# Performance work log

Hardware: AMD Instinct MI355X
Metric: run time of the kernel (lower is better)

## Reference

```python
import jax, jax.numpy as jnp
import numpy as np

N_NODES, N_EDGES, H, Q, RBF = 10000, 160000, 128, 16, 32
CUTOFF_UPPER = 4.5


def tensor_norm(t):
    # Frobenius norm squared over the trailing 3x3 dims -> [n, h]
    return (t * t).sum((-2, -1))


def decompose_tensor(X):
    # X: [n, h, 3, 3] -> I: [n, h] (trace/3), A skew, S symmetric-traceless
    eye = jnp.eye(3, dtype=X.dtype)
    I = jnp.einsum('nhii->nh', X) / 3.0
    Xt = jnp.swapaxes(X, -1, -2)
    A = 0.5 * (X - Xt)
    S = 0.5 * (X + Xt) - I[..., None, None] * eye
    return I, A, S


def I_to_tensor(I):
    return I[..., None, None] * jnp.eye(3, dtype=I.dtype)


def skewtensor_to_vector(A):
    return jnp.stack((A[..., 2, 1], A[..., 0, 2], A[..., 1, 0]), axis=-1)


def vector_to_skewtensor(v):
    z = jnp.zeros_like(v[..., 0])
    rows = jnp.stack((z, -v[..., 2], v[..., 1],
                      v[..., 2], z, -v[..., 0],
                      -v[..., 1], v[..., 0], z), axis=-1)
    return rows.reshape(v.shape[:-1] + (3, 3))


def setup_inputs() -> dict:
    key = jax.random.key(0)
    ks = jax.random.split(key, 12)
    d_in = RBF + 2 * Q  # 64
    inp = {
        'X': jax.random.normal(ks[0], (N_NODES, H, 3, 3), jnp.float32),
        'charges': jax.random.normal(ks[1], (N_NODES, Q), jnp.float32),
        'edge_weight': jax.random.uniform(ks[2], (N_EDGES,), jnp.float32) * CUTOFF_UPPER,
        'edge_attr': jax.random.normal(ks[3], (N_EDGES, RBF), jnp.float32),
        'W1': jax.random.normal(ks[4], (d_in, H), jnp.float32) / np.sqrt(d_in),
        'b1': jnp.zeros((H,), jnp.float32),
        'W2': jax.random.normal(ks[5], (H, 2 * H), jnp.float32) / np.sqrt(H),
        'b2': jnp.zeros((2 * H,), jnp.float32),
        'W3': jax.random.normal(ks[6], (2 * H, 3 * H), jnp.float32) / np.sqrt(2 * H),
        'b3': jnp.zeros((3 * H,), jnp.float32),
        'Wt': jax.random.normal(ks[7], (6, H, H), jnp.float32) / np.sqrt(H),
        'edge_index': jax.random.randint(ks[8], (2, N_EDGES), 0, N_NODES, jnp.int64 if jax.config.jax_enable_x64 else jnp.int32),
    }
    return inp


def reference(X, charges, edge_weight, edge_attr, W1, b1, W2, b2, W3, b3, Wt, edge_index):
    n, h = X.shape[0], X.shape[1]
    src, dst = edge_index[0], edge_index[1]

    # CosineCutoff (cutoff_lower = 0)
    C = 0.5 * (jnp.cos(edge_weight * (jnp.pi / CUTOFF_UPPER)) + 1.0)
    C = C * (edge_weight < CUTOFF_UPPER).astype(X.dtype)

    # edge MLP on [edge_attr | charges_i | charges_j]
    x = jnp.concatenate([edge_attr, charges[src], charges[dst]], axis=-1)
    x = jax.nn.silu(x @ W1 + b1)
    x = jax.nn.silu(x @ W2 + b2)
    x = jax.nn.silu(x @ W3 + b3)
    x = (x * C[:, None]).reshape(-1, 3, h)  # [E, 3, h]

    # normalize node tensor features
    X = X / (tensor_norm(X) + 1.0)[..., None, None]
    I, A, S = decompose_tensor(X)
    I = I @ Wt[0]
    A = jnp.einsum('nhij,hg->ngij', A, Wt[1])
    S = jnp.einsum('nhij,hg->ngij', S, Wt[2])
    Y = A + S + I_to_tensor(I)

    # message passing: gather from dst node, scale by edge factor, scatter-add to src
    Im = jax.ops.segment_sum(x[:, 0, :] * I[dst], src, num_segments=n)
    Av = skewtensor_to_vector(A)
    Am_vec = jax.ops.segment_sum(x[:, 1, :, None] * Av[dst], src, num_segments=n)
    Sm = jax.ops.segment_sum(x[:, 2, :, None, None] * S[dst], src, num_segments=n)
    msg = vector_to_skewtensor(Am_vec) + Sm + I_to_tensor(Im)

    # O(3) recombination
    A2 = jnp.matmul(msg, Y)
    B2 = jnp.matmul(Y, msg)
    I, A, S = decompose_tensor(A2 + B2)

    _X = A + S + I_to_tensor(I)
    normp1 = tensor_norm(_X) + 1.0
    I = I / normp1
    A = A / normp1[..., None, None]
    S = S / normp1[..., None, None]
    I = I @ Wt[3]
    A = jnp.einsum('nhij,hg->ngij', A, Wt[4])
    S = jnp.einsum('nhij,hg->ngij', S, Wt[5])
    dX = A + S + I_to_tensor(I)

    return X + dX + jnp.matmul(dX, dX)
```

## Files before the change

### kernel.cpp

```cpp
#include <hip/hip_runtime.h>
#include <math.h>

#define NND 10000
#define NE  160000
#define HD  128
#define NH  (NND*HD)

typedef _Float16 f16;
typedef _Float16 half8 __attribute__((ext_vector_type(8)));
typedef float floatx4 __attribute__((ext_vector_type(4)));

__device__ __forceinline__ float silu_f(float v) {
    return v * (1.0f / (1.0f + __expf(-v)));
}

__global__ __launch_bounds__(256) void w_prep(const float* __restrict__ W1,
                                              const float* __restrict__ W2,
                                              const float* __restrict__ W3,
                                              const float* __restrict__ Wt,
                                              f16* __restrict__ w1t,
                                              f16* __restrict__ w2t,
                                              f16* __restrict__ w3t,
                                              f16* __restrict__ wtT) {
    int id = blockIdx.x * 256 + threadIdx.x;
    if (id < 128*64) { int n = id >> 6, k = id & 63;  w1t[id] = (f16)W1[k*128 + n]; return; }
    id -= 128*64;
    if (id < 256*128) { int n = id >> 7, k = id & 127; w2t[id] = (f16)W2[k*256 + n]; return; }
    id -= 256*128;
    if (id < 384*256) { int n = id >> 8, k = id & 255; w3t[id] = (f16)W3[k*384 + n]; return; }
    id -= 384*256;
    if (id < 6*128*128) {
        int wi = id >> 14, rem = id & 16383;
        int n = rem >> 7, k = rem & 127;
        wtT[(size_t)wi*16384 + n*128 + k] = (f16)Wt[(size_t)wi*16384 + k*128 + n];
    }
}

__global__ __launch_bounds__(256) void hist_kernel(const int* __restrict__ eidx,
                                                   int* __restrict__ hist) {
    int e = blockIdx.x * 256 + threadIdx.x;
    if (e < NE) atomicAdd(&hist[eidx[e]], 1);
}

__global__ __launch_bounds__(1024) void scan_kernel(const int* __restrict__ hist,
                                                    int* __restrict__ offs,
                                                    int* __restrict__ cursor) {
    __shared__ int sums[1024];
    int t = threadIdx.x;
    int base = t * 10;
    int loc[10]; int s = 0;
    #pragma unroll
    for (int i = 0; i < 10; i++) {
        int v = (base + i < NND) ? hist[base + i] : 0;
        loc[i] = s; s += v;
    }
    sums[t] = s;
    __syncthreads();
    for (int off = 1; off < 1024; off <<= 1) {
        int v = (t >= off) ? sums[t - off] : 0;
        __syncthreads();
        sums[t] += v;
        __syncthreads();
    }
    int basesum = (t > 0) ? sums[t - 1] : 0;
    #pragma unroll
    for (int i = 0; i < 10; i++)
        if (base + i < NND) { offs[base + i] = basesum + loc[i]; cursor[base + i] = basesum + loc[i]; }
}

__global__ __launch_bounds__(256) void scatter_kernel(const int* __restrict__ eidx,
                                                      int* __restrict__ cursor,
                                                      int* __restrict__ perm,
                                                      int* __restrict__ ssrc,
                                                      int* __restrict__ sdst) {
    int e = blockIdx.x * 256 + threadIdx.x;
    if (e >= NE) return;
    int s = eidx[e], d = eidx[NE + e];
    int pos = atomicAdd(&cursor[s], 1);
    perm[pos] = e; ssrc[pos] = s; sdst[pos] = d;
}

__global__ __launch_bounds__(256) void node_prep(const float* __restrict__ X,
                                                 f16* __restrict__ comp) {
    int idx = blockIdx.x * 256 + threadIdx.x;
    if (idx >= NH) return;
    const float* xp = X + (size_t)idx * 9;
    float x[9];
    #pragma unroll
    for (int i = 0; i < 9; i++) x[i] = xp[i];
    float nsq = 0.f;
    #pragma unroll
    for (int i = 0; i < 9; i++) nsq = fmaf(x[i], x[i], nsq);
    float inv = 1.0f / (nsq + 1.0f);
    #pragma unroll
    for (int i = 0; i < 9; i++) x[i] *= inv;

    float I0  = (x[0] + x[4] + x[8]) * (1.0f / 3.0f);
    float a0  = 0.5f * (x[7] - x[5]);
    float a1  = 0.5f * (x[2] - x[6]);
    float a2  = 0.5f * (x[3] - x[1]);
    float s00 = x[0] - I0;
    float s11 = x[4] - I0;
    float s22 = x[8] - I0;
    float s01 = 0.5f * (x[1] + x[3]);
    float s02 = 0.5f * (x[2] + x[6]);
    float s12 = 0.5f * (x[5] + x[7]);

    comp[0*NH + idx] = (f16)I0;
    comp[1*NH + idx] = (f16)a0;  comp[2*NH + idx] = (f16)a1;  comp[3*NH + idx] = (f16)a2;
    comp[4*NH + idx] = (f16)s00; comp[5*NH + idx] = (f16)s11; comp[6*NH + idx] = (f16)s22;
    comp[7*NH + idx] = (f16)s01; comp[8*NH + idx] = (f16)s02; comp[9*NH + idx] = (f16)s12;
}

__global__ __launch_bounds__(256) void mix_mfma(const f16* __restrict__ A,
                                                const f16* __restrict__ WtT,
                                                float* __restrict__ C,
                                                f16* __restrict__ Ch,
                                                int w0, int w1, int w2, int writeCh) {
    const int g = blockIdx.y;
    const int baseRow = (g == 0) ? 0   : (g == 1 ? NND   : 4*NND);
    const int Mg      = (g == 0) ? NND : (g == 1 ? 3*NND : 6*NND);
    const int row0 = blockIdx.x * 64;
    if (row0 >= Mg) return;
    const int wi = (g == 0) ? w0 : (g == 1 ? w1 : w2);
    const f16* B = WtT + (size_t)wi * 128 * 128;

    __shared__ f16 As[64 * 136];

    const int t = threadIdx.x;
    const int l = t & 63, wid = t >> 6, lr = l & 15, lh = l >> 4;

    #pragma unroll
    for (int i = 0; i < 4; i++) {
        int id = t + 256 * i;
        int r = id >> 4, ch = id & 15;
        int rr = row0 + r; if (rr >= Mg) rr = Mg - 1;
        *(half8*)&As[r*136 + ch*8] =
            *(const half8*)&A[((size_t)baseRow + rr) * HD + ch*8];
    }
    __syncthreads();

    floatx4 acc[8];
    #pragma unroll
    for (int n = 0; n < 8; n++) acc[n] = (floatx4)0.0f;

    #pragma unroll
    for (int k0 = 0; k0 < 128; k0 += 32) {
        half8 a = *(const half8*)&As[(wid*16 + lr)*136 + k0 + lh*8];
        #pragma unroll
        for (int n = 0; n < 8; n++) {
            half8 b = *(const half8*)&B[(size_t)(n*16 + lr)*128 + k0 + lh*8];
            acc[n] = __builtin_amdgcn_mfma_f32_16x16x32_f16(a, b, acc[n], 0, 0, 0);
        }
    }

    #pragma unroll
    for (int n = 0; n < 8; n++) {
        #pragma unroll
        for (int r = 0; r < 4; r++) {
            int gl = row0 + wid*16 + lh*4 + r;
            if (gl < Mg) {
                size_t grow = (size_t)baseRow + gl;
                int col = n*16 + lr;
                float val = acc[n][r];
                C[grow * HD + col] = val;
                if (writeCh) {
                    int plane = (int)(grow / NND);
                    int node  = (int)(grow - (size_t)plane * NND);
                    Ch[((size_t)node * 10 + plane) * HD + col] = (f16)val;
                }
            }
        }
    }
}

__global__ __launch_bounds__(256, 3) void edge_mlp_v(
    const float* __restrict__ edge_attr, const float* __restrict__ charges,
    const float* __restrict__ edge_weight,
    const int* __restrict__ offs,
    const int* __restrict__ perm, const int* __restrict__ ssrc, const int* __restrict__ sdst,
    const f16* __restrict__ W1t, const float* __restrict__ b1,
    const f16* __restrict__ W2t, const float* __restrict__ b2,
    const f16* __restrict__ W3t, const float* __restrict__ b3,
    f16* __restrict__ vbuf, int n0, int n1, int VC)
{
    __shared__ __align__(16) char pool[51200];
    f16* x1s = (f16*)pool;
    f16* x2s = (f16*)(pool + 17408);
    f16* x0s = x2s;
    f16* stage = (f16*)pool;

    __shared__ int   srcS[64];
    __shared__ int   dstS[64];
    __shared__ int   permS[64];
    __shared__ float Cs[64];

    const int pbase = offs[n0];
    const int pend  = (n1 >= NND) ? NE : offs[n1];
    const int eb    = blockIdx.x * 64;
    if (pbase + eb >= pend) return;

    const int t   = threadIdx.x;
    const int l   = t & 63;
    const int wid = t >> 6;
    const int lr  = l & 15;
    const int lh  = l >> 4;

    if (t < 64) {
        int pe = pbase + eb + t;
        if (pe > NE - 1) pe = NE - 1;
        int eo = perm[pe];
        permS[t] = eo;
        srcS[t]  = ssrc[pe];
        dstS[t]  = sdst[pe];
        float w = edge_weight[eo];
        float c = 0.5f * (cosf(w * (float)(M_PI / 4.5)) + 1.0f);
        Cs[t] = (w < 4.5f) ? c : 0.0f;
    }
    __syncthreads();

    #pragma unroll
    for (int i = 0; i < 16; i++) {
        int lin = t + 256 * i;
        int e = lin >> 6, col = lin & 63;
        float v;
        if (col < 32)      v = edge_attr[(size_t)permS[e] * 32 + col];
        else if (col < 48) v = charges[(size_t)srcS[e] * 16 + (col - 32)];
        else               v = charges[(size_t)dstS[e] * 16 + (col - 48)];
        x0s[e * 72 + col] = (f16)v;
    }
    __syncthreads();

    {
        floatx4 acc[2][4];
        #pragma unroll
        for (int n = 0; n < 2; n++)
            #pragma unroll
            for (int m = 0; m < 4; m++) acc[n][m] = (floatx4)0.0f;

        #pragma unroll
        for (int k0 = 0; k0 < 64; k0 += 32) {
            half8 a[4];
            #pragma unroll
            for (int m = 0; m < 4; m++)
                a[m] = *(const half8*)&x0s[(m*16 + lr)*72 + k0 + lh*8];
            #pragma unroll
            for (int n = 0; n < 2; n++) {
                int colb = wid*32 + n*16 + lr;
                half8 b = *(const half8*)&W1t[(size_t)colb*64 + k0 + lh*8];
                #pragma unroll
                for (int m = 0; m < 4; m++)
                    acc[n][m] = __builtin_amdgcn_mfma_f32_16x16x32_f16(a[m], b, acc[n][m], 0, 0, 0);
            }
        }
        __syncthreads();
        #pragma unroll
        for (int n = 0; n < 2; n++) {
            int col = wid*32 + n*16 + lr;
            float bb = b1[col];
            #pragma unroll
            for (int m = 0; m < 4; m++)
                #pragma unroll
                for (int r = 0; r < 4; r++) {
                    int row = m*16 + lh*4 + r;
                    x1s[row*136 + col] = (f16)silu_f(acc[n][m][r] + bb);
                }
        }
    }
    __syncthreads();

    {
        floatx4 acc[4][4];
        #pragma unroll
        for (int n = 0; n < 4; n++)
            #pragma unroll
            for (int m = 0; m < 4; m++) acc[n][m] = (floatx4)0.0f;

        #pragma unroll
        for (int k0 = 0; k0 < 128; k0 += 32) {
            half8 a[4];
            #pragma unroll
            for (int m = 0; m < 4; m++)
                a[m] = *(const half8*)&x1s[(m*16 + lr)*136 + k0 + lh*8];
            #pragma unroll
            for (int n = 0; n < 4; n++) {
                int colb = wid*64 + n*16 + lr;
                half8 b = *(const half8*)&W2t[(size_t)colb*128 + k0 + lh*8];
                #pragma unroll
                for (int m = 0; m < 4; m++)
                    acc[n][m] = __builtin_amdgcn_mfma_f32_16x16x32_f16(a[m], b, acc[n][m], 0, 0, 0);
            }
        }
        #pragma unroll
        for (int n = 0; n < 4; n++) {
            int col = wid*64 + n*16 + lr;
            float bb = b2[col];
            #pragma unroll
            for (int m = 0; m < 4; m++)
                #pragma unroll
                for (int r = 0; r < 4; r++) {
                    int row = m*16 + lh*4 + r;
                    x2s[row*264 + col] = (f16)silu_f(acc[n][m][r] + bb);
                }
        }
    }
    __syncthreads();

    floatx4 acc[6][4];
    #pragma unroll
    for (int n = 0; n < 6; n++)
        #pragma unroll
        for (int m = 0; m < 4; m++) acc[n][m] = (floatx4)0.0f;

    #pragma unroll
    for (int k0 = 0; k0 < 256; k0 += 32) {
        half8 a[4];
        #pragma unroll
        for (int m = 0; m < 4; m++)
            a[m] = *(const half8*)&x2s[(m*16 + lr)*264 + k0 + lh*8];
        #pragma unroll
        for (int n = 0; n < 6; n++) {
            int colb = wid*96 + n*16 + lr;
            half8 b = *(const half8*)&W3t[(size_t)colb*256 + k0 + lh*8];
            #pragma unroll
            for (int m = 0; m < 4; m++)
                acc[n][m] = __builtin_amdgcn_mfma_f32_16x16x32_f16(a[m], b, acc[n][m], 0, 0, 0);
        }
    }
    __syncthreads();

    #pragma unroll
    for (int n = 0; n < 6; n++) {
        int col = wid*96 + n*16 + lr;
        int g = col >> 7, h = col & 127;
        float bb = b3[col];
        #pragma unroll
        for (int m = 0; m < 4; m++)
            #pragma unroll
            for (int r = 0; r < 4; r++) {
                int e = m*16 + lh*4 + r;
                stage[e*392 + g*128 + h] = (f16)(silu_f(acc[n][m][r] + bb) * Cs[e]);
            }
    }
    __syncthreads();

    #pragma unroll
    for (int i = 0; i < 12; i++) {
        int c = t + 256 * i;
        int e = c / 48, j = c - e * 48;
        int g = j >> 4, h0 = (j & 15) * 8;
        half8 v = *(const half8*)&stage[e*392 + j*8];
        *(half8*)&vbuf[((size_t)g*VC + (size_t)(eb + e))*HD + h0] = v;
    }
}

__global__ __launch_bounds__(128) void scatter_combine(
    const int* __restrict__ offs, const int* __restrict__ ends,
    const int* __restrict__ sdst, const f16* __restrict__ vbuf,
    const f16* __restrict__ Ych, const float* __restrict__ Yc,
    f16* __restrict__ pre, int n0, int VC)
{
    const int s = n0 + blockIdx.x;
    const int h = threadIdx.x;
    const int pbase = offs[n0];
    const int p0 = offs[s], p1 = ends[s];

    float ps[10];
    #pragma unroll
    for (int c = 0; c < 10; c++) ps[c] = 0.f;

    int p = p0;
    for (; p + 1 < p1; p += 2) {
        int sl0 = p - pbase, sl1 = sl0 + 1;
        int d0 = sdst[p], d1 = sdst[p + 1];
        const f16* y0 = Ych + (size_t)d0 * 1280 + h;
        const f16* y1 = Ych + (size_t)d1 * 1280 + h;
        float va0 = (float)vbuf[((size_t)0*VC + sl0)*HD + h];
        float vb0 = (float)vbuf[((size_t)1*VC + sl0)*HD + h];
        float vc0 = (float)vbuf[((size_t)2*VC + sl0)*HD + h];
        float va1 = (float)vbuf[((size_t)0*VC + sl1)*HD + h];
        float vb1 = (float)vbuf[((size_t)1*VC + sl1)*HD + h];
        float vc1 = (float)vbuf[((size_t)2*VC + sl1)*HD + h];
        float y0r[10], y1r[10];
        #pragma unroll
        for (int c = 0; c < 10; c++) { y0r[c] = (float)y0[c*HD]; y1r[c] = (float)y1[c*HD]; }
        ps[0] = fmaf(va0, y0r[0], ps[0]);
        #pragma unroll
        for (int c = 1; c < 4; c++)  ps[c] = fmaf(vb0, y0r[c], ps[c]);
        #pragma unroll
        for (int c = 4; c < 10; c++) ps[c] = fmaf(vc0, y0r[c], ps[c]);
        ps[0] = fmaf(va1, y1r[0], ps[0]);
        #pragma unroll
        for (int c = 1; c < 4; c++)  ps[c] = fmaf(vb1, y1r[c], ps[c]);
        #pragma unroll
        for (int c = 4; c < 10; c++) ps[c] = fmaf(vc1, y1r[c], ps[c]);
    }
    if (p < p1) {
        int sl0 = p - pbase;
        int d0 = sdst[p];
        const f16* y0 = Ych + (size_t)d0 * 1280 + h;
        float va0 = (float)vbuf[((size_t)0*VC + sl0)*HD + h];
        float vb0 = (float)vbuf[((size_t)1*VC + sl0)*HD + h];
        float vc0 = (float)vbuf[((size_t)2*VC + sl0)*HD + h];
        float y0r[10];
        #pragma unroll
        for (int c = 0; c < 10; c++) y0r[c] = (float)y0[c*HD];
        ps[0] = fmaf(va0, y0r[0], ps[0]);
        #pragma unroll
        for (int c = 1; c < 4; c++)  ps[c] = fmaf(vb0, y0r[c], ps[c]);
        #pragma unroll
        for (int c = 4; c < 10; c++) ps[c] = fmaf(vc0, y0r[c], ps[c]);
    }

    const size_t idx = (size_t)s * HD + h;
    float yI  = Yc[0*(size_t)NH + idx];
    float ya0 = Yc[1*(size_t)NH + idx], ya1 = Yc[2*(size_t)NH + idx], ya2 = Yc[3*(size_t)NH + idx];
    float ys00 = Yc[4*(size_t)NH + idx], ys11 = Yc[5*(size_t)NH + idx], ys22 = Yc[6*(size_t)NH + idx];
    float ys01 = Yc[7*(size_t)NH + idx], ys02 = Yc[8*(size_t)NH + idx], ys12 = Yc[9*(size_t)NH + idx];

    float M[3][3] = {
        { ps[0] + ps[4],  ps[7] - ps[3],  ps[8] + ps[2] },
        { ps[7] + ps[3],  ps[0] + ps[5],  ps[9] - ps[1] },
        { ps[8] - ps[2],  ps[9] + ps[1],  ps[0] + ps[6] } };
    float Y[3][3] = {
        { yI + ys00,  ys01 - ya2, ys02 + ya1 },
        { ys01 + ya2, yI + ys11,  ys12 - ya0 },
        { ys02 - ya1, ys12 + ya0, yI + ys22  } };

    float T[3][3];
    #pragma unroll
    for (int r = 0; r < 3; r++)
        #pragma unroll
        for (int c = 0; c < 3; c++) {
            float acc = 0.f;
            #pragma unroll
            for (int k = 0; k < 3; k++)
                acc += M[r][k] * Y[k][c] + Y[r][k] * M[k][c];
            T[r][c] = acc;
        }

    float tr3 = (T[0][0] + T[1][1] + T[2][2]) * (1.0f / 3.0f);
    float nsq = 0.f;
    #pragma unroll
    for (int r = 0; r < 3; r++)
        #pragma unroll
        for (int c = 0; c < 3; c++) nsq = fmaf(T[r][c], T[r][c], nsq);
    float inv = 1.0f / (nsq + 1.0f);

    pre[0*(size_t)NH + idx] = (f16)(tr3 * inv);
    pre[1*(size_t)NH + idx] = (f16)(0.5f * (T[2][1] - T[1][2]) * inv);
    pre[2*(size_t)NH + idx] = (f16)(0.5f * (T[0][2] - T[2][0]) * inv);
    pre[3*(size_t)NH + idx] = (f16)(0.5f * (T[1][0] - T[0][1]) * inv);
    pre[4*(size_t)NH + idx] = (f16)((T[0][0] - tr3) * inv);
    pre[5*(size_t)NH + idx] = (f16)((T[1][1] - tr3) * inv);
    pre[6*(size_t)NH + idx] = (f16)((T[2][2] - tr3) * inv);
    pre[7*(size_t)NH + idx] = (f16)(0.5f * (T[0][1] + T[1][0]) * inv);
    pre[8*(size_t)NH + idx] = (f16)(0.5f * (T[0][2] + T[2][0]) * inv);
    pre[9*(size_t)NH + idx] = (f16)(0.5f * (T[1][2] + T[2][1]) * inv);
}

__global__ __launch_bounds__(256) void final_out(const float* __restrict__ post,
                                                 const float* __restrict__ X,
                                                 float* __restrict__ out) {
    int idx = blockIdx.x * 256 + threadIdx.x;
    if (idx >= NH) return;

    float dI  = post[0*NH + idx];
    float da0 = post[1*NH + idx], da1 = post[2*NH + idx], da2 = post[3*NH + idx];
    float ds00 = post[4*NH + idx], ds11 = post[5*NH + idx], ds22 = post[6*NH + idx];
    float ds01 = post[7*NH + idx], ds02 = post[8*NH + idx], ds12 = post[9*NH + idx];

    float D[3][3] = {
        { dI + ds00,  ds01 - da2, ds02 + da1 },
        { ds01 + da2, dI + ds11,  ds12 - da0 },
        { ds02 - da1, ds12 + da0, dI + ds22  } };

    const float* xp = X + (size_t)idx * 9;
    float x[9];
    #pragma unroll
    for (int i = 0; i < 9; i++) x[i] = xp[i];
    float nsq = 0.f;
    #pragma unroll
    for (int i = 0; i < 9; i++) nsq = fmaf(x[i], x[i], nsq);
    float inv = 1.0f / (nsq + 1.0f);

    float* op = out + (size_t)idx * 9;
    #pragma unroll
    for (int r = 0; r < 3; r++)
        #pragma unroll
        for (int c = 0; c < 3; c++) {
            float p = 0.f;
            #pragma unroll
            for (int k = 0; k < 3; k++) p = fmaf(D[r][k], D[k][c], p);
            op[r*3 + c] = x[r*3 + c] * inv + D[r][c] + p;
        }
}

extern "C" void kernel_launch(void* const* d_in, const int* in_sizes, int n_in,
                              void* d_out, int out_size, void* d_ws, size_t ws_size,
                              hipStream_t stream) {
    const float* X       = (const float*)d_in[0];
    const float* charges = (const float*)d_in[1];
    const float* ew      = (const float*)d_in[2];
    const float* ea      = (const float*)d_in[3];
    const float* W1      = (const float*)d_in[4];
    const float* b1      = (const float*)d_in[5];
    const float* W2      = (const float*)d_in[6];
    const float* b2      = (const float*)d_in[7];
    const float* W3      = (const float*)d_in[8];
    const float* b3      = (const float*)d_in[9];
    const float* Wt      = (const float*)d_in[10];
    const int*   eidx    = (const int*)d_in[11];
    float* out = (float*)d_out;

    float* f32a  = (float*)d_ws;
    f16*   fh16  = (f16*)(f32a + (size_t)10 * NH);
    f16*   ych   = fh16 + (size_t)10 * NH;
    f16*   w1t   = ych + (size_t)10 * NH;
    f16*   w2t   = w1t + 128*64;
    f16*   w3t   = w2t + 256*128;
    f16*   wtT   = w3t + 384*256;
    int*   hist   = (int*)(wtT + 6*128*128);
    int*   offs   = hist + NND;
    int*   cursor = offs + NND;
    int*   perm   = cursor + NND;
    int*   ssrc   = perm + NE;
    int*   sdst   = ssrc + NE;
    f16*   vbuf   = (f16*)(sdst + NE);

    size_t used = (size_t)((char*)vbuf - (char*)d_ws);
    int Q, VC;
    if      (used + (size_t)160000 * 384 * 2 <= ws_size) { Q = 1; VC = 160000; }
    else if (used + (size_t) 84480 * 384 * 2 <= ws_size) { Q = 2; VC = 84480;  }
    else if (used + (size_t) 48000 * 384 * 2 <= ws_size) { Q = 4; VC = 48000;  }
    else                                                 { Q = 8; VC = 24320;  }

    hipMemsetAsync(hist, 0, NND * sizeof(int), stream);

    w_prep<<<928, 256, 0, stream>>>(W1, W2, W3, Wt, w1t, w2t, w3t, wtT);
    node_prep<<<NH / 256, 256, 0, stream>>>(X, fh16);

    hist_kernel<<<(NE + 255) / 256, 256, 0, stream>>>(eidx, hist);
    scan_kernel<<<1, 1024, 0, stream>>>(hist, offs, cursor);
    scatter_kernel<<<(NE + 255) / 256, 256, 0, stream>>>(eidx, cursor, perm, ssrc, sdst);

    dim3 gmix((6 * NND + 63) / 64, 3);
    mix_mfma<<<gmix, 256, 0, stream>>>(fh16, wtT, f32a, ych, 0, 1, 2, 1);

    const int nodesPer = NND / Q;
    for (int q = 0; q < Q; q++) {
        int n0 = q * nodesPer, n1 = n0 + nodesPer;
        edge_mlp_v<<<VC / 64, 256, 0, stream>>>(ea, charges, ew, offs,
                                                perm, ssrc, sdst,
                                                w1t, b1, w2t, b2, w3t, b3,
                                                vbuf, n0, n1, VC);
        scatter_combine<<<nodesPer, 128, 0, stream>>>(offs, cursor, sdst, vbuf,
                                                      ych, f32a, fh16, n0, VC);
    }

    mix_mfma<<<gmix, 256, 0, stream>>>(fh16, wtT, f32a, ych, 3, 4, 5, 0);

    final_out<<<NH / 256, 256, 0, stream>>>(f32a, X, out);
}
```

Measured before the change: 423.6 us.

## Shrink edge MLP tile to 32 edges, swap MFMA operands, interleave vbuf layout

The edge MLP kernel now processes 32 edges per block instead of 64. That halves shared memory and accumulator registers, so launch bounds can rise from 3 to 6 blocks per SM. MFMA operands are swapped so weights are the A operand, which lets epilogue stores and bias loads be written as 4-wide vectors. The input gather uses float4 loads, and vbuf switches from plane-major to per-edge interleaved 384-wide rows so edge writes and combine reads stay contiguous. The cost is half the weight reuse per block and twice as many blocks re-reading the W matrices from global or L2 memory.

```diff
diff --git a/kernel.cpp b/kernel.cpp
--- a/kernel.cpp
+++ b/kernel.cpp
@@ -8,6 +8,7 @@
 
 typedef _Float16 f16;
 typedef _Float16 half8 __attribute__((ext_vector_type(8)));
+typedef _Float16 half4 __attribute__((ext_vector_type(4)));
 typedef float floatx4 __attribute__((ext_vector_type(4)));
 
 __device__ __forceinline__ float silu_f(float v) {
@@ -174,7 +175,7 @@
     }
 }
 
-__global__ __launch_bounds__(256, 3) void edge_mlp_v(
+__global__ __launch_bounds__(256, 6) void edge_mlp_v(
     const float* __restrict__ edge_attr, const float* __restrict__ charges,
     const float* __restrict__ edge_weight,
     const int* __restrict__ offs,
@@ -184,20 +185,20 @@
     const f16* __restrict__ W3t, const float* __restrict__ b3,
     f16* __restrict__ vbuf, int n0, int n1, int VC)
 {
-    __shared__ __align__(16) char pool[51200];
+    __shared__ __align__(16) char pool[25600];
     f16* x1s = (f16*)pool;
-    f16* x2s = (f16*)(pool + 17408);
+    f16* x2s = (f16*)(pool + 8704);
     f16* x0s = x2s;
     f16* stage = (f16*)pool;
 
-    __shared__ int   srcS[64];
-    __shared__ int   dstS[64];
-    __shared__ int   permS[64];
-    __shared__ float Cs[64];
+    __shared__ int   srcS[32];
+    __shared__ int   dstS[32];
+    __shared__ int   permS[32];
+    __shared__ float Cs[32];
 
     const int pbase = offs[n0];
     const int pend  = (n1 >= NND) ? NE : offs[n1];
-    const int eb    = blockIdx.x * 64;
+    const int eb    = blockIdx.x * 32;
     if (pbase + eb >= pend) return;
 
     const int t   = threadIdx.x;
@@ -206,7 +207,7 @@
     const int lr  = l & 15;
     const int lh  = l >> 4;
 
-    if (t < 64) {
+    if (t < 32) {
         int pe = pbase + eb + t;
         if (pe > NE - 1) pe = NE - 1;
         int eo = perm[pe];
@@ -219,138 +220,144 @@
     }
     __syncthreads();
 
-    #pragma unroll
-    for (int i = 0; i < 16; i++) {
-        int lin = t + 256 * i;
-        int e = lin >> 6, col = lin & 63;
-        float v;
-        if (col < 32)      v = edge_attr[(size_t)permS[e] * 32 + col];
-        else if (col < 48) v = charges[(size_t)srcS[e] * 16 + (col - 32)];
-        else               v = charges[(size_t)dstS[e] * 16 + (col - 48)];
-        x0s[e * 72 + col] = (f16)v;
-    }
-    __syncthreads();
-
     {
-        floatx4 acc[2][4];
+        int e = t >> 3, q = t & 7;
+        float4 va = *(const float4*)&edge_attr[(size_t)permS[e] * 32 + q * 4];
+        half4 ha; ha[0]=(f16)va.x; ha[1]=(f16)va.y; ha[2]=(f16)va.z; ha[3]=(f16)va.w;
+        *(half4*)&x0s[e*72 + q*4] = ha;
+        float4 vc; int col;
+        if (q < 4) { vc = *(const float4*)&charges[(size_t)srcS[e]*16 + q*4]; col = 32 + q*4; }
+        else       { vc = *(const float4*)&charges[(size_t)dstS[e]*16 + (q-4)*4]; col = 48 + (q-4)*4; }
+        half4 hc; hc[0]=(f16)vc.x; hc[1]=(f16)vc.y; hc[2]=(f16)vc.z; hc[3]=(f16)vc.w;
+        *(half4*)&x0s[e*72 + col] = hc;
+    }
+    __syncthreads();
+
+    {
+        floatx4 acc[2][2];
         #pragma unroll
         for (int n = 0; n < 2; n++)
             #pragma unroll
-            for (int m = 0; m < 4; m++) acc[n][m] = (floatx4)0.0f;
+            for (int m = 0; m < 2; m++) acc[n][m] = (floatx4)0.0f;
 
         #pragma unroll
         for (int k0 = 0; k0 < 64; k0 += 32) {
-            half8 a[4];
-            #pragma unroll
-            for (int m = 0; m < 4; m++)
-                a[m] = *(const half8*)&x0s[(m*16 + lr)*72 + k0 + lh*8];
+            half8 b[2];
+            #pragma unroll
+            for (int m = 0; m < 2; m++)
+                b[m] = *(const half8*)&x0s[(m*16 + lr)*72 + k0 + lh*8];
             #pragma unroll
             for (int n = 0; n < 2; n++) {
-                int colb = wid*32 + n*16 + lr;
-                half8 b = *(const half8*)&W1t[(size_t)colb*64 + k0 + lh*8];
+                half8 a = *(const half8*)&W1t[(size_t)(wid*32 + n*16 + lr)*64 + k0 + lh*8];
                 #pragma unroll
-                for (int m = 0; m < 4; m++)
-                    acc[n][m] = __builtin_amdgcn_mfma_f32_16x16x32_f16(a[m], b, acc[n][m], 0, 0, 0);
+                for (int m = 0; m < 2; m++)
+                    acc[n][m] = __builtin_amdgcn_mfma_f32_16x16x32_f16(a, b[m], acc[n][m], 0, 0, 0);
             }
         }
         __syncthreads();
         #pragma unroll
         for (int n = 0; n < 2; n++) {
-            int col = wid*32 + n*16 + lr;
-            float bb = b1[col];
-            #pragma unroll
-            for (int m = 0; m < 4; m++)
+            int col0 = wid*32 + n*16 + lh*4;
+            float4 bb = *(const float4*)&b1[col0];
+            #pragma unroll
+            for (int m = 0; m < 2; m++) {
+                int e = m*16 + lr;
+                half4 hv;
+                hv[0] = (f16)silu_f(acc[n][m][0] + bb.x);
+                hv[1] = (f16)silu_f(acc[n][m][1] + bb.y);
+                hv[2] = (f16)silu_f(acc[n][m][2] + bb.z);
+                hv[3] = (f16)silu_f(acc[n][m][3] + bb.w);
+                *(half4*)&x1s[e*136 + col0] = hv;
+            }
+        }
+    }
+    __syncthreads();
+
+    {
+        floatx4 acc[4][2];
+        #pragma unroll
+        for (int n = 0; n < 4; n++)
+            #pragma unroll
+            for (int m = 0; m < 2; m++) acc[n][m] = (floatx4)0.0f;
+
+        #pragma unroll
+        for (int k0 = 0; k0 < 128; k0 += 32) {
+            half8 b[2];
+            #pragma unroll
+            for (int m = 0; m < 2; m++)
+                b[m] = *(const half8*)&x1s[(m*16 + lr)*136 + k0 + lh*8];
+            #pragma unroll
+            for (int n = 0; n < 4; n++) {
+                half8 a = *(const half8*)&W2t[(size_t)(wid*64 + n*16 + lr)*128 + k0 + lh*8];
                 #pragma unroll
-                for (int r = 0; r < 4; r++) {
-                    int row = m*16 + lh*4 + r;
-                    x1s[row*136 + col] = (f16)silu_f(acc[n][m][r] + bb);
-                }
-        }
-    }
-    __syncthreads();
-
-    {
-        floatx4 acc[4][4];
-        #pragma unroll
-        for (int n = 0; n < 4; n++)
-            #pragma unroll
-            for (int m = 0; m < 4; m++) acc[n][m] = (floatx4)0.0f;
-
-        #pragma unroll
-        for (int k0 = 0; k0 < 128; k0 += 32) {
-            half8 a[4];
-            #pragma unroll
-            for (int m = 0; m < 4; m++)
-                a[m] = *(const half8*)&x1s[(m*16 + lr)*136 + k0 + lh*8];
-            #pragma unroll
-            for (int n = 0; n < 4; n++) {
-                int colb = wid*64 + n*16 + lr;
-                half8 b = *(const half8*)&W2t[(size_t)colb*128 + k0 + lh*8];
-                #pragma unroll
-                for (int m = 0; m < 4; m++)
-                    acc[n][m] = __builtin_amdgcn_mfma_f32_16x16x32_f16(a[m], b, acc[n][m], 0, 0, 0);
+                for (int m = 0; m < 2; m++)
+                    acc[n][m] = __builtin_amdgcn_mfma_f32_16x16x32_f16(a, b[m], acc[n][m], 0, 0, 0);
             }
         }
         #pragma unroll
         for (int n = 0; n < 4; n++) {
-            int col = wid*64 + n*16 + lr;
-            float bb = b2[col];
-            #pragma unroll
-            for (int m = 0; m < 4; m++)
-                #pragma unroll
-                for (int r = 0; r < 4; r++) {
-                    int row = m*16 + lh*4 + r;
-                    x2s[row*264 + col] = (f16)silu_f(acc[n][m][r] + bb);
-                }
-        }
-    }
-    __syncthreads();
-
-    floatx4 acc[6][4];
+            int col0 = wid*64 + n*16 + lh*4;
+            float4 bb = *(const float4*)&b2[col0];
+            #pragma unroll
+            for (int m = 0; m < 2; m++) {
+                int e = m*16 + lr;
+                half4 hv;
+                hv[0] = (f16)silu_f(acc[n][m][0] + bb.x);
+                hv[1] = (f16)silu_f(acc[n][m][1] + bb.y);
+                hv[2] = (f16)silu_f(acc[n][m][2] + bb.z);
+                hv[3] = (f16)silu_f(acc[n][m][3] + bb.w);
+                *(half4*)&x2s[e*264 + col0] = hv;
+            }
+        }
+    }
+    __syncthreads();
+
+    floatx4 acc[6][2];
     #pragma unroll
     for (int n = 0; n < 6; n++)
         #pragma unroll
-        for (int m = 0; m < 4; m++) acc[n][m] = (floatx4)0.0f;
+        for (int m = 0; m < 2; m++) acc[n][m] = (floatx4)0.0f;
 
     #pragma unroll
     for (int k0 = 0; k0 < 256; k0 += 32) {
-        half8 a[4];
-        #pragma unroll
-        for (int m = 0; m < 4; m++)
-            a[m] = *(const half8*)&x2s[(m*16 + lr)*264 + k0 + lh*8];
+        half8 b[2];
+        #pragma unroll
+        for (int m = 0; m < 2; m++)
+            b[m] = *(const half8*)&x2s[(m*16 + lr)*264 + k0 + lh*8];
         #pragma unroll
         for (int n = 0; n < 6; n++) {
-            int colb = wid*96 + n*16 + lr;
-            half8 b = *(const half8*)&W3t[(size_t)colb*256 + k0 + lh*8];
-            #pragma unroll
-            for (int m = 0; m < 4; m++)
-                acc[n][m] = __builtin_amdgcn_mfma_f32_16x16x32_f16(a[m], b, acc[n][m], 0, 0, 0);
+            half8 a = *(const half8*)&W3t[(size_t)(wid*96 + n*16 + lr)*256 + k0 + lh*8];
+            #pragma unroll
+            for (int m = 0; m < 2; m++)
+                acc[n][m] = __builtin_amdgcn_mfma_f32_16x16x32_f16(a, b[m], acc[n][m], 0, 0, 0);
         }
     }
     __syncthreads();
 
     #pragma unroll
     for (int n = 0; n < 6; n++) {
-        int col = wid*96 + n*16 + lr;
-        int g = col >> 7, h = col & 127;
-        float bb = b3[col];
-        #pragma unroll
-        for (int m = 0; m < 4; m++)
-            #pragma unroll
-            for (int r = 0; r < 4; r++) {
-                int e = m*16 + lh*4 + r;
-                stage[e*392 + g*128 + h] = (f16)(silu_f(acc[n][m][r] + bb) * Cs[e]);
-            }
-    }
-    __syncthreads();
-
-    #pragma unroll
-    for (int i = 0; i < 12; i++) {
+        int col0 = wid*96 + n*16 + lh*4;
+        float4 bb = *(const float4*)&b3[col0];
+        #pragma unroll
+        for (int m = 0; m < 2; m++) {
+            int e = m*16 + lr;
+            float cf = Cs[e];
+            half4 hv;
+            hv[0] = (f16)(silu_f(acc[n][m][0] + bb.x) * cf);
+            hv[1] = (f16)(silu_f(acc[n][m][1] + bb.y) * cf);
+            hv[2] = (f16)(silu_f(acc[n][m][2] + bb.z) * cf);
+            hv[3] = (f16)(silu_f(acc[n][m][3] + bb.w) * cf);
+            *(half4*)&stage[e*392 + col0] = hv;
+        }
+    }
+    __syncthreads();
+
+    #pragma unroll
+    for (int i = 0; i < 6; i++) {
         int c = t + 256 * i;
         int e = c / 48, j = c - e * 48;
-        int g = j >> 4, h0 = (j & 15) * 8;
         half8 v = *(const half8*)&stage[e*392 + j*8];
-        *(half8*)&vbuf[((size_t)g*VC + (size_t)(eb + e))*HD + h0] = v;
+        *(half8*)&vbuf[(size_t)(eb + e) * 384 + j*8] = v;
     }
 }
 
@@ -375,12 +382,12 @@
         int d0 = sdst[p], d1 = sdst[p + 1];
         const f16* y0 = Ych + (size_t)d0 * 1280 + h;
         const f16* y1 = Ych + (size_t)d1 * 1280 + h;
-        float va0 = (float)vbuf[((size_t)0*VC + sl0)*HD + h];
-        float vb0 = (float)vbuf[((size_t)1*VC + sl0)*HD + h];
-        float vc0 = (float)vbuf[((size_t)2*VC + sl0)*HD + h];
-        float va1 = (float)vbuf[((size_t)0*VC + sl1)*HD + h];
-        float vb1 = (float)vbuf[((size_t)1*VC + sl1)*HD + h];
-        float vc1 = (float)vbuf[((size_t)2*VC + sl1)*HD + h];
+        float va0 = (float)vbuf[(size_t)sl0*384 + h];
+        float vb0 = (float)vbuf[(size_t)sl0*384 + 128 + h];
+        float vc0 = (float)vbuf[(size_t)sl0*384 + 256 + h];
+        float va1 = (float)vbuf[(size_t)sl1*384 + h];
+        float vb1 = (float)vbuf[(size_t)sl1*384 + 128 + h];
+        float vc1 = (float)vbuf[(size_t)sl1*384 + 256 + h];
         float y0r[10], y1r[10];
         #pragma unroll
         for (int c = 0; c < 10; c++) { y0r[c] = (float)y0[c*HD]; y1r[c] = (float)y1[c*HD]; }
@@ -399,9 +406,9 @@
         int sl0 = p - pbase;
         int d0 = sdst[p];
         const f16* y0 = Ych + (size_t)d0 * 1280 + h;
-        float va0 = (float)vbuf[((size_t)0*VC + sl0)*HD + h];
-        float vb0 = (float)vbuf[((size_t)1*VC + sl0)*HD + h];
-        float vc0 = (float)vbuf[((size_t)2*VC + sl0)*HD + h];
+        float va0 = (float)vbuf[(size_t)sl0*384 + h];
+        float vb0 = (float)vbuf[(size_t)sl0*384 + 128 + h];
+        float vc0 = (float)vbuf[(size_t)sl0*384 + 256 + h];
         float y0r[10];
         #pragma unroll
         for (int c = 0; c < 10; c++) y0r[c] = (float)y0[c*HD];
@@ -550,7 +557,7 @@
     const int nodesPer = NND / Q;
     for (int q = 0; q < Q; q++) {
         int n0 = q * nodesPer, n1 = n0 + nodesPer;
-        edge_mlp_v<<<VC / 64, 256, 0, stream>>>(ea, charges, ew, offs,
+        edge_mlp_v<<<VC / 32, 256, 0, stream>>>(ea, charges, ew, offs,
                                                 perm, ssrc, sdst,
                                                 w1t, b1, w2t, b2, w3t, b3,
                                                 vbuf, n0, n1, VC);
```

Measured after the change: 455.7 us. +7.6%, slower.

## Split fused edge MLP into three per-layer GEMM kernels with global intermediates

Applied to the files above, without the earlier changes.

Replaces the single fused three-layer edge MLP kernel with three separate kernels, each handling one layer and passing fp16 activations through global buffers. The smaller per-kernel LDS and register footprint is meant to raise occupancy, and it adds vectorized input loads. The output vbuf layout changes from plane-major to edge-major with 384 values per edge, and scatter_combine reads are adjusted to match. The cost is extra global traffic for the intermediates (about 768 bytes per edge written and read back), two extra launches per chunk, and a larger workspace requirement.

```diff
diff --git a/kernel.cpp b/kernel.cpp
--- a/kernel.cpp
+++ b/kernel.cpp
@@ -8,6 +8,7 @@
 
 typedef _Float16 f16;
 typedef _Float16 half8 __attribute__((ext_vector_type(8)));
+typedef _Float16 half4 __attribute__((ext_vector_type(4)));
 typedef float floatx4 __attribute__((ext_vector_type(4)));
 
 __device__ __forceinline__ float silu_f(float v) {
@@ -174,183 +175,220 @@
     }
 }
 
-__global__ __launch_bounds__(256, 3) void edge_mlp_v(
+__global__ __launch_bounds__(256, 6) void edge_gemm1(
     const float* __restrict__ edge_attr, const float* __restrict__ charges,
-    const float* __restrict__ edge_weight,
     const int* __restrict__ offs,
     const int* __restrict__ perm, const int* __restrict__ ssrc, const int* __restrict__ sdst,
     const f16* __restrict__ W1t, const float* __restrict__ b1,
-    const f16* __restrict__ W2t, const float* __restrict__ b2,
-    const f16* __restrict__ W3t, const float* __restrict__ b3,
-    f16* __restrict__ vbuf, int n0, int n1, int VC)
+    f16* __restrict__ x1b, int n0, int n1)
 {
-    __shared__ __align__(16) char pool[51200];
-    f16* x1s = (f16*)pool;
-    f16* x2s = (f16*)(pool + 17408);
-    f16* x0s = x2s;
-    f16* stage = (f16*)pool;
-
-    __shared__ int   srcS[64];
-    __shared__ int   dstS[64];
-    __shared__ int   permS[64];
-    __shared__ float Cs[64];
+    __shared__ f16 As[64 * 72];
+    __shared__ int srcS[64], dstS[64], permS[64];
 
     const int pbase = offs[n0];
     const int pend  = (n1 >= NND) ? NE : offs[n1];
     const int eb    = blockIdx.x * 64;
     if (pbase + eb >= pend) return;
 
-    const int t   = threadIdx.x;
-    const int l   = t & 63;
-    const int wid = t >> 6;
-    const int lr  = l & 15;
-    const int lh  = l >> 4;
+    const int t = threadIdx.x;
+    const int l = t & 63, wid = t >> 6, lr = l & 15, lh = l >> 4;
 
     if (t < 64) {
         int pe = pbase + eb + t;
         if (pe > NE - 1) pe = NE - 1;
-        int eo = perm[pe];
-        permS[t] = eo;
+        permS[t] = perm[pe];
         srcS[t]  = ssrc[pe];
         dstS[t]  = sdst[pe];
-        float w = edge_weight[eo];
+    }
+    __syncthreads();
+
+    {
+        int e = t >> 2, q = t & 3;
+        #pragma unroll
+        for (int jj = 0; jj < 2; jj++) {
+            int j = q + jj*4;
+            float4 va = *(const float4*)&edge_attr[(size_t)permS[e]*32 + j*4];
+            half4 hv; hv[0]=(f16)va.x; hv[1]=(f16)va.y; hv[2]=(f16)va.z; hv[3]=(f16)va.w;
+            *(half4*)&As[e*72 + j*4] = hv;
+        }
+        int node = (q < 2) ? srcS[e] : dstS[e];
+        int qq   = (q < 2) ? q : (q - 2);
+        int cb   = (q < 2) ? 32 : 48;
+        #pragma unroll
+        for (int jj = 0; jj < 2; jj++) {
+            int j = qq + jj*2;
+            float4 vc = *(const float4*)&charges[(size_t)node*16 + j*4];
+            half4 hv; hv[0]=(f16)vc.x; hv[1]=(f16)vc.y; hv[2]=(f16)vc.z; hv[3]=(f16)vc.w;
+            *(half4*)&As[e*72 + cb + j*4] = hv;
+        }
+    }
+    __syncthreads();
+
+    floatx4 acc[2][4];
+    #pragma unroll
+    for (int n = 0; n < 2; n++)
+        #pragma unroll
+        for (int m = 0; m < 4; m++) acc[n][m] = (floatx4)0.0f;
+
+    #pragma unroll
+    for (int k0 = 0; k0 < 64; k0 += 32) {
+        half8 a[4];
+        #pragma unroll
+        for (int m = 0; m < 4; m++)
+            a[m] = *(const half8*)&As[(m*16 + lr)*72 + k0 + lh*8];
+        #pragma unroll
+        for (int n = 0; n < 2; n++) {
+            half8 b = *(const half8*)&W1t[(size_t)(wid*32 + n*16 + lr)*64 + k0 + lh*8];
+            #pragma unroll
+            for (int m = 0; m < 4; m++)
+                acc[n][m] = __builtin_amdgcn_mfma_f32_16x16x32_f16(a[m], b, acc[n][m], 0, 0, 0);
+        }
+    }
+
+    #pragma unroll
+    for (int n = 0; n < 2; n++) {
+        int col = wid*32 + n*16 + lr;
+        float bb = b1[col];
+        #pragma unroll
+        for (int m = 0; m < 4; m++)
+            #pragma unroll
+            for (int r = 0; r < 4; r++) {
+                int e = m*16 + lh*4 + r;
+                x1b[(size_t)(eb + e)*128 + col] = (f16)silu_f(acc[n][m][r] + bb);
+            }
+    }
+}
+
+__global__ __launch_bounds__(256, 4) void edge_gemm2(
+    const int* __restrict__ offs,
+    const f16* __restrict__ x1b,
+    const f16* __restrict__ W2t, const float* __restrict__ b2,
+    f16* __restrict__ x2b, int n0, int n1)
+{
+    __shared__ f16 As[64 * 136];
+
+    const int pbase = offs[n0];
+    const int pend  = (n1 >= NND) ? NE : offs[n1];
+    const int eb    = blockIdx.x * 64;
+    if (pbase + eb >= pend) return;
+
+    const int t = threadIdx.x;
+    const int l = t & 63, wid = t >> 6, lr = l & 15, lh = l >> 4;
+
+    #pragma unroll
+    for (int i = 0; i < 4; i++) {
+        int id = t + 256 * i;
+        int r = id >> 4, c = id & 15;
+        *(half8*)&As[r*136 + c*8] = *(const half8*)&x1b[(size_t)(eb + r)*128 + c*8];
+    }
+    __syncthreads();
+
+    floatx4 acc[4][4];
+    #pragma unroll
+    for (int n = 0; n < 4; n++)
+        #pragma unroll
+        for (int m = 0; m < 4; m++) acc[n][m] = (floatx4)0.0f;
+
+    #pragma unroll
+    for (int k0 = 0; k0 < 128; k0 += 32) {
+        half8 a[4];
+        #pragma unroll
+        for (int m = 0; m < 4; m++)
+            a[m] = *(const half8*)&As[(m*16 + lr)*136 + k0 + lh*8];
+        #pragma unroll
+        for (int n = 0; n < 4; n++) {
+            half8 b = *(const half8*)&W2t[(size_t)(wid*64 + n*16 + lr)*128 + k0 + lh*8];
+            #pragma unroll
+            for (int m = 0; m < 4; m++)
+                acc[n][m] = __builtin_amdgcn_mfma_f32_16x16x32_f16(a[m], b, acc[n][m], 0, 0, 0);
+        }
+    }
+
+    #pragma unroll
+    for (int n = 0; n < 4; n++) {
+        int col = wid*64 + n*16 + lr;
+        float bb = b2[col];
+        #pragma unroll
+        for (int m = 0; m < 4; m++)
+            #pragma unroll
+            for (int r = 0; r < 4; r++) {
+                int e = m*16 + lh*4 + r;
+                x2b[(size_t)(eb + e)*256 + col] = (f16)silu_f(acc[n][m][r] + bb);
+            }
+    }
+}
+
+__global__ __launch_bounds__(256, 3) void edge_gemm3(
+    const float* __restrict__ edge_weight,
+    const int* __restrict__ offs, const int* __restrict__ perm,
+    const f16* __restrict__ x2b,
+    const f16* __restrict__ W3t, const float* __restrict__ b3,
+    f16* __restrict__ vbuf, int n0, int n1)
+{
+    __shared__ f16 As[64 * 136];
+    __shared__ float Cs[64];
+
+    const int pbase = offs[n0];
+    const int pend  = (n1 >= NND) ? NE : offs[n1];
+    const int eb    = blockIdx.x * 64;
+    if (pbase + eb >= pend) return;
+
+    const int t = threadIdx.x;
+    const int l = t & 63, wid = t >> 6, lr = l & 15, lh = l >> 4;
+
+    if (t < 64) {
+        int pe = pbase + eb + t;
+        if (pe > NE - 1) pe = NE - 1;
+        float w = edge_weight[perm[pe]];
         float c = 0.5f * (cosf(w * (float)(M_PI / 4.5)) + 1.0f);
         Cs[t] = (w < 4.5f) ? c : 0.0f;
     }
-    __syncthreads();
-
-    #pragma unroll
-    for (int i = 0; i < 16; i++) {
-        int lin = t + 256 * i;
-        int e = lin >> 6, col = lin & 63;
-        float v;
-        if (col < 32)      v = edge_attr[(size_t)permS[e] * 32 + col];
-        else if (col < 48) v = charges[(size_t)srcS[e] * 16 + (col - 32)];
-        else               v = charges[(size_t)dstS[e] * 16 + (col - 48)];
-        x0s[e * 72 + col] = (f16)v;
-    }
-    __syncthreads();
-
-    {
-        floatx4 acc[2][4];
-        #pragma unroll
-        for (int n = 0; n < 2; n++)
-            #pragma unroll
-            for (int m = 0; m < 4; m++) acc[n][m] = (floatx4)0.0f;
-
-        #pragma unroll
-        for (int k0 = 0; k0 < 64; k0 += 32) {
+
+    floatx4 acc[6][4];
+    #pragma unroll
+    for (int n = 0; n < 6; n++)
+        #pragma unroll
+        for (int m = 0; m < 4; m++) acc[n][m] = (floatx4)0.0f;
+
+    #pragma unroll
+    for (int kb = 0; kb < 2; kb++) {
+        __syncthreads();
+        #pragma unroll
+        for (int i = 0; i < 4; i++) {
+            int id = t + 256 * i;
+            int r = id >> 4, c = id & 15;
+            *(half8*)&As[r*136 + c*8] =
+                *(const half8*)&x2b[(size_t)(eb + r)*256 + kb*128 + c*8];
+        }
+        __syncthreads();
+
+        #pragma unroll
+        for (int k0 = 0; k0 < 128; k0 += 32) {
             half8 a[4];
             #pragma unroll
             for (int m = 0; m < 4; m++)
-                a[m] = *(const half8*)&x0s[(m*16 + lr)*72 + k0 + lh*8];
-            #pragma unroll
-            for (int n = 0; n < 2; n++) {
-                int colb = wid*32 + n*16 + lr;
-                half8 b = *(const half8*)&W1t[(size_t)colb*64 + k0 + lh*8];
+                a[m] = *(const half8*)&As[(m*16 + lr)*136 + k0 + lh*8];
+            #pragma unroll
+            for (int n = 0; n < 6; n++) {
+                half8 b = *(const half8*)&W3t[(size_t)(wid*96 + n*16 + lr)*256 + kb*128 + k0 + lh*8];
                 #pragma unroll
                 for (int m = 0; m < 4; m++)
                     acc[n][m] = __builtin_amdgcn_mfma_f32_16x16x32_f16(a[m], b, acc[n][m], 0, 0, 0);
             }
         }
-        __syncthreads();
-        #pragma unroll
-        for (int n = 0; n < 2; n++) {
-            int col = wid*32 + n*16 + lr;
-            float bb = b1[col];
-            #pragma unroll
-            for (int m = 0; m < 4; m++)
-                #pragma unroll
-                for (int r = 0; r < 4; r++) {
-                    int row = m*16 + lh*4 + r;
-                    x1s[row*136 + col] = (f16)silu_f(acc[n][m][r] + bb);
-                }
-        }
-    }
-    __syncthreads();
-
-    {
-        floatx4 acc[4][4];
-        #pragma unroll
-        for (int n = 0; n < 4; n++)
-            #pragma unroll
-            for (int m = 0; m < 4; m++) acc[n][m] = (floatx4)0.0f;
-
-        #pragma unroll
-        for (int k0 = 0; k0 < 128; k0 += 32) {
-            half8 a[4];
-            #pragma unroll
-            for (int m = 0; m < 4; m++)
-                a[m] = *(const half8*)&x1s[(m*16 + lr)*136 + k0 + lh*8];
-            #pragma unroll
-            for (int n = 0; n < 4; n++) {
-                int colb = wid*64 + n*16 + lr;
-                half8 b = *(const half8*)&W2t[(size_t)colb*128 + k0 + lh*8];
-                #pragma unroll
-                for (int m = 0; m < 4; m++)
-                    acc[n][m] = __builtin_amdgcn_mfma_f32_16x16x32_f16(a[m], b, acc[n][m], 0, 0, 0);
-            }
-        }
-        #pragma unroll
-        for (int n = 0; n < 4; n++) {
-            int col = wid*64 + n*16 + lr;
-            float bb = b2[col];
-            #pragma unroll
-            for (int m = 0; m < 4; m++)
-                #pragma unroll
-                for (int r = 0; r < 4; r++) {
-                    int row = m*16 + lh*4 + r;
-                    x2s[row*264 + col] = (f16)silu_f(acc[n][m][r] + bb);
-                }
-        }
-    }
-    __syncthreads();
-
-    floatx4 acc[6][4];
-    #pragma unroll
-    for (int n = 0; n < 6; n++)
-        #pragma unroll
-        for (int m = 0; m < 4; m++) acc[n][m] = (floatx4)0.0f;
-
-    #pragma unroll
-    for (int k0 = 0; k0 < 256; k0 += 32) {
-        half8 a[4];
-        #pragma unroll
-        for (int m = 0; m < 4; m++)
-            a[m] = *(const half8*)&x2s[(m*16 + lr)*264 + k0 + lh*8];
-        #pragma unroll
-        for (int n = 0; n < 6; n++) {
-            int colb = wid*96 + n*16 + lr;
-            half8 b = *(const half8*)&W3t[(size_t)colb*256 + k0 + lh*8];
-            #pragma unroll
-            for (int m = 0; m < 4; m++)
-                acc[n][m] = __builtin_amdgcn_mfma_f32_16x16x32_f16(a[m], b, acc[n][m], 0, 0, 0);
-        }
-    }
-    __syncthreads();
+    }
 
     #pragma unroll
     for (int n = 0; n < 6; n++) {
         int col = wid*96 + n*16 + lr;
-        int g = col >> 7, h = col & 127;
         float bb = b3[col];
         #pragma unroll
         for (int m = 0; m < 4; m++)
             #pragma unroll
             for (int r = 0; r < 4; r++) {
                 int e = m*16 + lh*4 + r;
-                stage[e*392 + g*128 + h] = (f16)(silu_f(acc[n][m][r] + bb) * Cs[e]);
+                vbuf[(size_t)(eb + e)*384 + col] = (f16)(silu_f(acc[n][m][r] + bb) * Cs[e]);
             }
-    }
-    __syncthreads();
-
-    #pragma unroll
-    for (int i = 0; i < 12; i++) {
-        int c = t + 256 * i;
-        int e = c / 48, j = c - e * 48;
-        int g = j >> 4, h0 = (j & 15) * 8;
-        half8 v = *(const half8*)&stage[e*392 + j*8];
-        *(half8*)&vbuf[((size_t)g*VC + (size_t)(eb + e))*HD + h0] = v;
     }
 }
 
@@ -375,12 +413,12 @@
         int d0 = sdst[p], d1 = sdst[p + 1];
         const f16* y0 = Ych + (size_t)d0 * 1280 + h;
         const f16* y1 = Ych + (size_t)d1 * 1280 + h;
-        float va0 = (float)vbuf[((size_t)0*VC + sl0)*HD + h];
-        float vb0 = (float)vbuf[((size_t)1*VC + sl0)*HD + h];
-        float vc0 = (float)vbuf[((size_t)2*VC + sl0)*HD + h];
-        float va1 = (float)vbuf[((size_t)0*VC + sl1)*HD + h];
-        float vb1 = (float)vbuf[((size_t)1*VC + sl1)*HD + h];
-        float vc1 = (float)vbuf[((size_t)2*VC + sl1)*HD + h];
+        float va0 = (float)vbuf[(size_t)sl0*384 + h];
+        float vb0 = (float)vbuf[(size_t)sl0*384 + 128 + h];
+        float vc0 = (float)vbuf[(size_t)sl0*384 + 256 + h];
+        float va1 = (float)vbuf[(size_t)sl1*384 + h];
+        float vb1 = (float)vbuf[(size_t)sl1*384 + 128 + h];
+        float vc1 = (float)vbuf[(size_t)sl1*384 + 256 + h];
         float y0r[10], y1r[10];
         #pragma unroll
         for (int c = 0; c < 10; c++) { y0r[c] = (float)y0[c*HD]; y1r[c] = (float)y1[c*HD]; }
@@ -399,9 +437,9 @@
         int sl0 = p - pbase;
         int d0 = sdst[p];
         const f16* y0 = Ych + (size_t)d0 * 1280 + h;
-        float va0 = (float)vbuf[((size_t)0*VC + sl0)*HD + h];
-        float vb0 = (float)vbuf[((size_t)1*VC + sl0)*HD + h];
-        float vc0 = (float)vbuf[((size_t)2*VC + sl0)*HD + h];
+        float va0 = (float)vbuf[(size_t)sl0*384 + h];
+        float vb0 = (float)vbuf[(size_t)sl0*384 + 128 + h];
+        float vc0 = (float)vbuf[(size_t)sl0*384 + 256 + h];
         float y0r[10];
         #pragma unroll
         for (int c = 0; c < 10; c++) y0r[c] = (float)y0[c*HD];
@@ -530,10 +568,12 @@
 
     size_t used = (size_t)((char*)vbuf - (char*)d_ws);
     int Q, VC;
-    if      (used + (size_t)160000 * 384 * 2 <= ws_size) { Q = 1; VC = 160000; }
-    else if (used + (size_t) 84480 * 384 * 2 <= ws_size) { Q = 2; VC = 84480;  }
-    else if (used + (size_t) 48000 * 384 * 2 <= ws_size) { Q = 4; VC = 48000;  }
-    else                                                 { Q = 8; VC = 24320;  }
+    if      (used + (size_t)160000 * 1536 <= ws_size) { Q = 1; VC = 160000; }
+    else if (used + (size_t) 84480 * 1536 <= ws_size) { Q = 2; VC = 84480;  }
+    else if (used + (size_t) 48000 * 1536 <= ws_size) { Q = 4; VC = 48000;  }
+    else                                              { Q = 8; VC = 24320;  }
+    f16* x1b = vbuf + (size_t)VC * 384;
+    f16* x2b = x1b  + (size_t)VC * 128;
 
     hipMemsetAsync(hist, 0, NND * sizeof(int), stream);
 
@@ -550,10 +590,12 @@
     const int nodesPer = NND / Q;
     for (int q = 0; q < Q; q++) {
         int n0 = q * nodesPer, n1 = n0 + nodesPer;
-        edge_mlp_v<<<VC / 64, 256, 0, stream>>>(ea, charges, ew, offs,
-                                                perm, ssrc, sdst,
-                                                w1t, b1, w2t, b2, w3t, b3,
-                                                vbuf, n0, n1, VC);
+        int nb = VC / 64;
+        edge_gemm1<<<nb, 256, 0, stream>>>(ea, charges, offs, perm, ssrc, sdst,
+                                           w1t, b1, x1b, n0, n1);
+        edge_gemm2<<<nb, 256, 0, stream>>>(offs, x1b, w2t, b2, x2b, n0, n1);
+        edge_gemm3<<<nb, 256, 0, stream>>>(ew, offs, perm, x2b, w3t, b3,
+                                           vbuf, n0, n1);
         scatter_combine<<<nodesPer, 128, 0, stream>>>(offs, cursor, sdst, vbuf,
                                                       ych, f32a, fh16, n0, VC);
     }
```

New measurement: 460.5 us. +8.7%, slower.
